# Performance work log

Hardware: AMD Instinct MI355X
Metric: run time of the kernel (lower is better)

Reference implementation:

```python
import jax, jax.numpy as jnp
from jax import lax
import numpy as np

T, N, E = 4, 50000, 1600000
IN_CH, HID, OUT = 128, 128, 16


def setup_inputs() -> dict:
    key = jax.random.key(0)
    ks = jax.random.split(key, 10)
    s = lambda fan: 1.0 / np.sqrt(fan)
    return {
        "xs": jax.random.normal(ks[0], (T, N, IN_CH), jnp.float32),
        "edges": jax.random.randint(ks[1], (T, 2, E), 0, N, dtype=jnp.int32),
        "W_gcn": jax.random.normal(ks[2], (HID, IN_CH), jnp.float32) * s(IN_CH),
        "b_gcn": jax.random.normal(ks[3], (HID,), jnp.float32) * s(IN_CH),
        "W_ih": jax.random.normal(ks[4], (3 * HID, HID), jnp.float32) * s(HID),
        "W_hh": jax.random.normal(ks[5], (3 * HID, HID), jnp.float32) * s(HID),
        "b_ih": jax.random.normal(ks[6], (3 * HID,), jnp.float32) * s(HID),
        "b_hh": jax.random.normal(ks[7], (3 * HID,), jnp.float32) * s(HID),
        "W_cls": jax.random.normal(ks[8], (OUT, HID), jnp.float32) * s(HID),
        "b_cls": jax.random.normal(ks[9], (OUT,), jnp.float32) * s(HID),
    }


def reference(xs, edges, W_gcn, b_gcn, W_ih, W_hh, b_ih, b_hh, W_cls, b_cls):
    n = xs.shape[1]
    loop = jnp.arange(n, dtype=edges.dtype)

    def gcn_forward(x, ei):
        src = jnp.concatenate([ei[0], loop])  # add self loops
        dst = jnp.concatenate([ei[1], loop])
        h = x @ W_gcn.T + b_gcn                               # [N, H]
        agg = jax.ops.segment_sum(h[src], dst, num_segments=n)  # scatter_add features
        deg = jax.ops.segment_sum(jnp.ones(dst.shape[0], h.dtype), dst, num_segments=n)
        return jax.nn.relu(agg / jnp.maximum(deg, 1.0)[:, None])

    def gru_cell(z, h):
        gi = z @ W_ih.T + b_ih   # [1, 3H]
        gh = h @ W_hh.T + b_hh
        ir, iz, ig = jnp.split(gi, 3, axis=1)
        hr, hz, hg = jnp.split(gh, 3, axis=1)
        r = jax.nn.sigmoid(ir + hr)
        zg = jax.nn.sigmoid(iz + hz)
        ng = jnp.tanh(ig + r * hg)
        return (1.0 - zg) * ng + zg * h

    def step(h, snap):
        x, ei = snap
        z_mean = gcn_forward(x, ei).mean(axis=0, keepdims=True)  # [1, H]
        return gru_cell(z_mean, h), None

    h0 = jnp.zeros((1, W_hh.shape[1]), xs.dtype)
    h, _ = lax.scan(step, h0, (xs, edges))
    return h @ W_cls.T + b_cls  # [1, OUT]
```

## Files before the change

kernel.cpp:

```cpp
#include <hip/hip_runtime.h>
#include <hip/hip_bf16.h>

typedef unsigned int u32;
typedef unsigned short u16;
typedef unsigned char u8;
typedef __attribute__((ext_vector_type(8))) __bf16 bfrag;
typedef __attribute__((ext_vector_type(4))) float f32x4;
typedef __attribute__((ext_vector_type(2))) float f32x2;

#define T_STEPS 4
#define N_NODES 50000
#define E_EDGES 1600000
#define HID 128
#define OUT_CH 16

#define NCHUNK 128
#define CHUNK (E_EDGES / NCHUNK)
#define NBKT 196
#define BCAP 10240

#define H_STRIDE    6400000u
#define RS_STRIDE   204800u
#define ZP_STRIDE   16384u
#define CSR_STRIDE  3200000u

#define OFF_H     0u
#define OFF_RS    25600000u
#define OFF_ZPAD  26419200u
#define OFF_CSR   26484736u
#define OFF_WB    39284736u
#define OFF_GCNT  39317504u
#define OFF_BBASE 39321600u
#define OFF_RECS  39325696u

__device__ __forceinline__ u8 f32_to_fp8(float v) {
    return (u8)(__builtin_amdgcn_cvt_pk_fp8_f32(v, v, 0, 0) & 0xFF);
}

__global__ void wbf_kernel(const float* __restrict__ W, __bf16* __restrict__ wb) {
    const int i = blockIdx.x * 256 + threadIdx.x;
    wb[i] = (__bf16)W[i];
}

__global__ __launch_bounds__(256) void gemm_mfma_kernel(const float* __restrict__ xs,
                                                        const __bf16* __restrict__ wb,
                                                        const float* __restrict__ b,
                                                        u8* __restrict__ h8_all) {
    const int lane = threadIdx.x & 63;
    const int wv   = threadIdx.x >> 6;
    const int r16  = lane & 15;
    const int quad = lane >> 4;
    const int mb   = blockIdx.x;
    const int t    = blockIdx.y;
    const float* x = xs + (size_t)t * N_NODES * 128;
    u8* h8         = h8_all + (size_t)t * H_STRIDE;

    bfrag Bf[2][4];
#pragma unroll
    for (int nt = 0; nt < 2; ++nt) {
        const int c = wv * 32 + nt * 16 + r16;
#pragma unroll
        for (int ks = 0; ks < 4; ++ks)
            Bf[nt][ks] = *(const bfrag*)(wb + c * 128 + ks * 32 + quad * 8);
    }

    const float* xp = x + (size_t)(mb * 16 + r16) * 128 + quad * 8;
    bfrag Af[4];
#pragma unroll
    for (int ks = 0; ks < 4; ++ks) {
        const float* ap = xp + ks * 32;
#pragma unroll
        for (int j = 0; j < 8; ++j) Af[ks][j] = (__bf16)ap[j];
    }

    f32x4 acc0 = {0.f, 0.f, 0.f, 0.f};
    f32x4 acc1 = {0.f, 0.f, 0.f, 0.f};
#pragma unroll
    for (int ks = 0; ks < 4; ++ks) {
        acc0 = __builtin_amdgcn_mfma_f32_16x16x32_bf16(Af[ks], Bf[0][ks], acc0, 0, 0, 0);
        acc1 = __builtin_amdgcn_mfma_f32_16x16x32_bf16(Af[ks], Bf[1][ks], acc1, 0, 0, 0);
    }

    const int c0 = wv * 32 + r16;
    const float b0 = b[c0], b1 = b[c0 + 16];
#pragma unroll
    for (int r = 0; r < 4; ++r) {
        const size_t row = (size_t)(mb * 16 + quad * 4 + r) * 128;
        h8[row + c0]      = f32_to_fp8(acc0[r] + b0);
        h8[row + c0 + 16] = f32_to_fp8(acc1[r] + b1);
    }
}

__global__ __launch_bounds__(256) void part_kernel(const int* __restrict__ edges,
                                                   u32* __restrict__ gcnt,
                                                   u32* __restrict__ recs) {
    __shared__ u32 bh[NBKT], bc[NBKT];
    const int id  = blockIdx.x;
    const int xcd = id & 7;
    const int t   = xcd >> 1;
    const int c   = ((xcd & 1) << 6) | (id >> 3);
    const int base = c * CHUNK;
    const int* src = edges + (size_t)t * 2 * E_EDGES;
    const int* dst = src + E_EDGES;
    u32* rt = recs + (size_t)t * NBKT * BCAP;
    const int tid = threadIdx.x;

    if (tid < NBKT) bh[tid] = 0;
    __syncthreads();
    for (int i = tid; i < CHUNK; i += 256)
        atomicAdd(&bh[dst[base + i] >> 8], 1u);
    __syncthreads();
    if (tid < NBKT) bc[tid] = atomicAdd(&gcnt[t * 256 + tid], bh[tid]);
    __syncthreads();
    for (int i = tid; i < CHUNK; i += 256) {
        const int d = dst[base + i];
        const int s = src[base + i];
        const int bkt = d >> 8;
        const u32 idx = atomicAdd(&bc[bkt], 1u);
        if (idx < (u32)BCAP)
            rt[(size_t)bkt * BCAP + idx] = ((u32)(d & 255) << 16) | (u32)s;
    }
}

__global__ __launch_bounds__(256) void bscan_kernel(const u32* __restrict__ gcnt,
                                                    u32* __restrict__ bbase) {
    __shared__ u32 sc[256];
    const int tid = threadIdx.x;
    for (int t = 0; t < T_STEPS; ++t) {
        u32 v = (tid < NBKT) ? min(gcnt[t * 256 + tid], (u32)BCAP) : 0u;
        const u32 mine = v;
        sc[tid] = v;
        __syncthreads();
        for (int d = 1; d < 256; d <<= 1) {
            const u32 u = (tid >= d) ? sc[tid - d] : 0u;
            __syncthreads();
            sc[tid] += u;
            __syncthreads();
        }
        if (tid < NBKT) bbase[t * 256 + tid] = sc[tid] - mine;
        __syncthreads();
    }
}

__global__ __launch_bounds__(256) void build_kernel(const u32* __restrict__ recs,
                                                    const u32* __restrict__ gcnt,
                                                    const u32* __restrict__ bbase,
                                                    int* __restrict__ rs_all,
                                                    u16* __restrict__ csr_all) {
    __shared__ u32 ncnt[256];
    __shared__ u32 ncur[256];
    __shared__ u16 cl[BCAP];
    const int id  = blockIdx.x;
    const int xcd = id & 7;
    const int t   = xcd >> 1;
    const int b   = ((xcd & 1) ? 98 : 0) + (id >> 3);
    const int tid = threadIdx.x;
    const u32 cnt   = min(gcnt[t * 256 + b], (u32)BCAP);
    const u32 rbase = bbase[t * 256 + b];
    const u32* rp = recs + ((size_t)t * NBKT + b) * BCAP;
    int* rs  = rs_all + (size_t)t * (RS_STRIDE / 4);
    u16* csr = csr_all + (size_t)t * (CSR_STRIDE / 2);

    ncnt[tid] = 0;
    __syncthreads();
    for (u32 i = tid; i < cnt; i += 256)
        atomicAdd(&ncnt[rp[i] >> 16], 1u);
    __syncthreads();
    const u32 mine = ncnt[tid];
    for (int d = 1; d < 256; d <<= 1) {
        const u32 v = (tid >= d) ? ncnt[tid - d] : 0u;
        __syncthreads();
        ncnt[tid] += v;
        __syncthreads();
    }
    const u32 off = ncnt[tid] - mine;
    ncur[tid] = off;
    const int n = b * 256 + tid;
    if (n <= N_NODES) rs[n] = (int)(rbase + off);
    __syncthreads();
    for (u32 i = tid; i < cnt; i += 256) {
        const u32 r = rp[i];
        const u32 p = atomicAdd(&ncur[r >> 16], 1u);
        cl[p] = (u16)(r & 0xFFFFu);
    }
    __syncthreads();
    for (u32 i = tid; i < cnt; i += 256)
        csr[rbase + i] = cl[i];
}

__global__ __launch_bounds__(256) void gather_kernel(const u32* __restrict__ h8_all,
                                                     const int* __restrict__ rs_all,
                                                     const u16* __restrict__ csr_all,
                                                     float* __restrict__ zp_all) {
    const int lane = threadIdx.x & 63;
    const int wv   = __builtin_amdgcn_readfirstlane((int)(threadIdx.x >> 6));
    const int q    = lane & 31;
    const bool h0  = lane < 32;
    const int o    = h0 ? 0 : 1;
    const int id   = blockIdx.x;
    const int xcd  = id & 7;
    const int t    = xcd >> 1;
    const int kb   = ((xcd & 1) << 10) | (id >> 3);
    const u32* h8d = h8_all + (size_t)t * (H_STRIDE / 4);
    const int* row_start = rs_all + (size_t)t * (RS_STRIDE / 4);
    const u16* csr = csr_all + (size_t)t * (CSR_STRIDE / 2);
    float* z_pad = zp_all + (size_t)t * (ZP_STRIDE / 4);
    const int gw   = kb * 4 + wv;
    const int nw   = 2048 * 4;

    float z0 = 0.f, z1 = 0.f, z2 = 0.f, z3 = 0.f;
    for (int n = gw; n < N_NODES; n += nw) {
        const int rs  = row_start[n];
        const int cnt = row_start[n + 1] - rs;
        const u32 us = h8d[n * 32 + q];
        const f32x2 slo = __builtin_amdgcn_cvt_pk_f32_fp8(us, 0);
        const f32x2 shi = __builtin_amdgcn_cvt_pk_f32_fp8(us, 1);
        float a0 = h0 ? slo.x : 0.f;
        float a1 = h0 ? slo.y : 0.f;
        float a2 = h0 ? shi.x : 0.f;
        float a3 = h0 ? shi.y : 0.f;

        const u16* lst = csr + rs;
        int i = 0;
        for (; i + 8 <= cnt; i += 8) {
            const int s0 = lst[i + 0 + o];
            const int s1 = lst[i + 2 + o];
            const int s2 = lst[i + 4 + o];
            const int s3 = lst[i + 6 + o];
            const u32 u0 = h8d[s0 * 32 + q];
            const u32 u1 = h8d[s1 * 32 + q];
            const u32 u2 = h8d[s2 * 32 + q];
            const u32 u3 = h8d[s3 * 32 + q];
            const f32x2 l0 = __builtin_amdgcn_cvt_pk_f32_fp8(u0, 0);
            const f32x2 g0 = __builtin_amdgcn_cvt_pk_f32_fp8(u0, 1);
            const f32x2 l1 = __builtin_amdgcn_cvt_pk_f32_fp8(u1, 0);
            const f32x2 g1 = __builtin_amdgcn_cvt_pk_f32_fp8(u1, 1);
            const f32x2 l2 = __builtin_amdgcn_cvt_pk_f32_fp8(u2, 0);
            const f32x2 g2 = __builtin_amdgcn_cvt_pk_f32_fp8(u2, 1);
            const f32x2 l3 = __builtin_amdgcn_cvt_pk_f32_fp8(u3, 0);
            const f32x2 g3 = __builtin_amdgcn_cvt_pk_f32_fp8(u3, 1);
            a0 += (l0.x + l1.x) + (l2.x + l3.x);
            a1 += (l0.y + l1.y) + (l2.y + l3.y);
            a2 += (g0.x + g1.x) + (g2.x + g3.x);
            a3 += (g0.y + g1.y) + (g2.y + g3.y);
        }
        for (; i + 2 <= cnt; i += 2) {
            const int s = lst[i + o];
            const u32 u = h8d[s * 32 + q];
            const f32x2 lo = __builtin_amdgcn_cvt_pk_f32_fp8(u, 0);
            const f32x2 hi = __builtin_amdgcn_cvt_pk_f32_fp8(u, 1);
            a0 += lo.x; a1 += lo.y; a2 += hi.x; a3 += hi.y;
        }
        if (i < cnt) {
            const int s = lst[i];
            const u32 u = h8d[s * 32 + q];
            const f32x2 lo = __builtin_amdgcn_cvt_pk_f32_fp8(u, 0);
            const f32x2 hi = __builtin_amdgcn_cvt_pk_f32_fp8(u, 1);
            if (h0) { a0 += lo.x; a1 += lo.y; a2 += hi.x; a3 += hi.y; }
        }
        a0 += __shfl_xor(a0, 32);
        a1 += __shfl_xor(a1, 32);
        a2 += __shfl_xor(a2, 32);
        a3 += __shfl_xor(a3, 32);
        const float inv = 1.0f / (float)(cnt + 1);
        z0 += fmaxf(a0 * inv, 0.f);
        z1 += fmaxf(a1 * inv, 0.f);
        z2 += fmaxf(a2 * inv, 0.f);
        z3 += fmaxf(a3 * inv, 0.f);
    }

    __shared__ float red[4][64][4];
    red[wv][lane][0] = z0;
    red[wv][lane][1] = z1;
    red[wv][lane][2] = z2;
    red[wv][lane][3] = z3;
    __syncthreads();
    if (threadIdx.x < 128) {
        const int c = threadIdx.x;
        const int g = c >> 2, m = c & 3;
        float s = 0.f;
#pragma unroll
        for (int w = 0; w < 4; ++w) s += red[w][g][m] + red[w][g + 32][m];
        atomicAdd(&z_pad[c * 32], 0.5f * s);
    }
}

__global__ __launch_bounds__(512) void gru_all_kernel(const float* __restrict__ zp_all,
                                                      const float* __restrict__ W_ih,
                                                      const float* __restrict__ W_hh,
                                                      const float* __restrict__ b_ih,
                                                      const float* __restrict__ b_hh,
                                                      const float* __restrict__ W_cls,
                                                      const float* __restrict__ b_cls,
                                                      float* __restrict__ out) {
    __shared__ float zm[128], hs[128], gi[384], gh[384];
    const int tid = threadIdx.x;
    if (tid < 128) hs[tid] = 0.f;
    for (int t = 0; t < T_STEPS; ++t) {
        if (tid < 128)
            zm[tid] = zp_all[(size_t)t * (ZP_STRIDE / 4) + tid * 32] * (1.0f / (float)N_NODES);
        __syncthreads();
        if (tid < 384) {
            float a = b_ih[tid], g = b_hh[tid];
            const float* wi = W_ih + tid * 128;
            const float* wh = W_hh + tid * 128;
#pragma unroll 8
            for (int k = 0; k < 128; ++k) {
                a = fmaf(zm[k], wi[k], a);
                g = fmaf(hs[k], wh[k], g);
            }
            gi[tid] = a;
            gh[tid] = g;
        }
        __syncthreads();
        if (tid < 128) {
            const float r  = 1.f / (1.f + expf(-(gi[tid] + gh[tid])));
            const float zg = 1.f / (1.f + expf(-(gi[128 + tid] + gh[128 + tid])));
            const float ng = tanhf(gi[256 + tid] + r * gh[256 + tid]);
            hs[tid] = (1.f - zg) * ng + zg * hs[tid];
        }
        __syncthreads();
    }
    if (tid < OUT_CH) {
        float a = b_cls[tid];
        const float* wc = W_cls + tid * 128;
#pragma unroll 8
        for (int k = 0; k < 128; ++k) a = fmaf(hs[k], wc[k], a);
        out[tid] = a;
    }
}

extern "C" void kernel_launch(void* const* d_in, const int* in_sizes, int n_in,
                              void* d_out, int out_size, void* d_ws, size_t ws_size,
                              hipStream_t stream) {
    const float* xs    = (const float*)d_in[0];
    const int*   edges = (const int*)d_in[1];
    const float* W_gcn = (const float*)d_in[2];
    const float* b_gcn = (const float*)d_in[3];
    const float* W_ih  = (const float*)d_in[4];
    const float* W_hh  = (const float*)d_in[5];
    const float* b_ih  = (const float*)d_in[6];
    const float* b_hh  = (const float*)d_in[7];
    const float* W_cls = (const float*)d_in[8];
    const float* b_cls = (const float*)d_in[9];
    float* out = (float*)d_out;

    char* ws = (char*)d_ws;
    u8*    h8        = (u8*)(ws + OFF_H);
    int*   row_start = (int*)(ws + OFF_RS);
    float* z_pad     = (float*)(ws + OFF_ZPAD);
    u16*   csr       = (u16*)(ws + OFF_CSR);
    __bf16* wb       = (__bf16*)(ws + OFF_WB);
    u32*   gcnt      = (u32*)(ws + OFF_GCNT);
    u32*   bbase     = (u32*)(ws + OFF_BBASE);
    u32*   recs      = (u32*)(ws + OFF_RECS);

    hipMemsetAsync(z_pad, 0, 4 * ZP_STRIDE, stream);
    hipMemsetAsync(gcnt, 0, 4096, stream);
    wbf_kernel<<<64, 256, 0, stream>>>(W_gcn, wb);

    gemm_mfma_kernel<<<dim3(3125, T_STEPS), 256, 0, stream>>>(xs, wb, b_gcn, h8);
    part_kernel<<<NCHUNK * T_STEPS, 256, 0, stream>>>(edges, gcnt, recs);
    bscan_kernel<<<1, 256, 0, stream>>>(gcnt, bbase);
    build_kernel<<<98 * 8, 256, 0, stream>>>(recs, gcnt, bbase, row_start, csr);
    gather_kernel<<<2048 * T_STEPS, 256, 0, stream>>>((const u32*)h8, row_start, csr, z_pad);
    gru_all_kernel<<<1, 512, 0, stream>>>(z_pad, W_ih, W_hh, b_ih, b_hh,
                                          W_cls, b_cls, out);
}
```

Measured before the change: 568.2 us.

## Split feature dimension across XCD halves and gather four edges per wave

```diff
diff --git a/kernel.cpp b/kernel.cpp
--- a/kernel.cpp
+++ b/kernel.cpp
@@ -194,43 +194,44 @@
                                                      float* __restrict__ zp_all) {
     const int lane = threadIdx.x & 63;
     const int wv   = __builtin_amdgcn_readfirstlane((int)(threadIdx.x >> 6));
-    const int q    = lane & 31;
-    const bool h0  = lane < 32;
-    const int o    = h0 ? 0 : 1;
+    const int qh   = lane & 15;
+    const int quar = lane >> 4;
     const int id   = blockIdx.x;
     const int xcd  = id & 7;
     const int t    = xcd >> 1;
-    const int kb   = ((xcd & 1) << 10) | (id >> 3);
-    const u32* h8d = h8_all + (size_t)t * (H_STRIDE / 4);
+    const int half = xcd & 1;
+    const int kb   = id >> 3;
+    const u32* h8d = h8_all + (size_t)t * (H_STRIDE / 4) + half * 16;
     const int* row_start = rs_all + (size_t)t * (RS_STRIDE / 4);
     const u16* csr = csr_all + (size_t)t * (CSR_STRIDE / 2);
     float* z_pad = zp_all + (size_t)t * (ZP_STRIDE / 4);
     const int gw   = kb * 4 + wv;
-    const int nw   = 2048 * 4;
+    const int nw   = 1024 * 4;
 
     float z0 = 0.f, z1 = 0.f, z2 = 0.f, z3 = 0.f;
     for (int n = gw; n < N_NODES; n += nw) {
         const int rs  = row_start[n];
         const int cnt = row_start[n + 1] - rs;
-        const u32 us = h8d[n * 32 + q];
+        const u32 us = h8d[n * 32 + qh];
         const f32x2 slo = __builtin_amdgcn_cvt_pk_f32_fp8(us, 0);
         const f32x2 shi = __builtin_amdgcn_cvt_pk_f32_fp8(us, 1);
-        float a0 = h0 ? slo.x : 0.f;
-        float a1 = h0 ? slo.y : 0.f;
-        float a2 = h0 ? shi.x : 0.f;
-        float a3 = h0 ? shi.y : 0.f;
+        const bool q0 = (quar == 0);
+        float a0 = q0 ? slo.x : 0.f;
+        float a1 = q0 ? slo.y : 0.f;
+        float a2 = q0 ? shi.x : 0.f;
+        float a3 = q0 ? shi.y : 0.f;
 
         const u16* lst = csr + rs;
         int i = 0;
-        for (; i + 8 <= cnt; i += 8) {
-            const int s0 = lst[i + 0 + o];
-            const int s1 = lst[i + 2 + o];
-            const int s2 = lst[i + 4 + o];
-            const int s3 = lst[i + 6 + o];
-            const u32 u0 = h8d[s0 * 32 + q];
-            const u32 u1 = h8d[s1 * 32 + q];
-            const u32 u2 = h8d[s2 * 32 + q];
-            const u32 u3 = h8d[s3 * 32 + q];
+        for (; i + 16 <= cnt; i += 16) {
+            const int s0 = lst[i + 0  + quar];
+            const int s1 = lst[i + 4  + quar];
+            const int s2 = lst[i + 8  + quar];
+            const int s3 = lst[i + 12 + quar];
+            const u32 u0 = h8d[s0 * 32 + qh];
+            const u32 u1 = h8d[s1 * 32 + qh];
+            const u32 u2 = h8d[s2 * 32 + qh];
+            const u32 u3 = h8d[s3 * 32 + qh];
             const f32x2 l0 = __builtin_amdgcn_cvt_pk_f32_fp8(u0, 0);
             const f32x2 g0 = __builtin_amdgcn_cvt_pk_f32_fp8(u0, 1);
             const f32x2 l1 = __builtin_amdgcn_cvt_pk_f32_fp8(u1, 0);
@@ -244,24 +245,24 @@
             a2 += (g0.x + g1.x) + (g2.x + g3.x);
             a3 += (g0.y + g1.y) + (g2.y + g3.y);
         }
-        for (; i + 2 <= cnt; i += 2) {
-            const int s = lst[i + o];
-            const u32 u = h8d[s * 32 + q];
+        for (; i + 4 <= cnt; i += 4) {
+            const int s = lst[i + quar];
+            const u32 u = h8d[s * 32 + qh];
             const f32x2 lo = __builtin_amdgcn_cvt_pk_f32_fp8(u, 0);
             const f32x2 hi = __builtin_amdgcn_cvt_pk_f32_fp8(u, 1);
             a0 += lo.x; a1 += lo.y; a2 += hi.x; a3 += hi.y;
         }
-        if (i < cnt) {
-            const int s = lst[i];
-            const u32 u = h8d[s * 32 + q];
+        if (quar < cnt - i) {
+            const int s = lst[i + quar];
+            const u32 u = h8d[s * 32 + qh];
             const f32x2 lo = __builtin_amdgcn_cvt_pk_f32_fp8(u, 0);
             const f32x2 hi = __builtin_amdgcn_cvt_pk_f32_fp8(u, 1);
-            if (h0) { a0 += lo.x; a1 += lo.y; a2 += hi.x; a3 += hi.y; }
-        }
-        a0 += __shfl_xor(a0, 32);
-        a1 += __shfl_xor(a1, 32);
-        a2 += __shfl_xor(a2, 32);
-        a3 += __shfl_xor(a3, 32);
+            a0 += lo.x; a1 += lo.y; a2 += hi.x; a3 += hi.y;
+        }
+        a0 += __shfl_xor(a0, 16); a0 += __shfl_xor(a0, 32);
+        a1 += __shfl_xor(a1, 16); a1 += __shfl_xor(a1, 32);
+        a2 += __shfl_xor(a2, 16); a2 += __shfl_xor(a2, 32);
+        a3 += __shfl_xor(a3, 16); a3 += __shfl_xor(a3, 32);
         const float inv = 1.0f / (float)(cnt + 1);
         z0 += fmaxf(a0 * inv, 0.f);
         z1 += fmaxf(a1 * inv, 0.f);
@@ -269,19 +270,21 @@
         z3 += fmaxf(a3 * inv, 0.f);
     }
 
-    __shared__ float red[4][64][4];
-    red[wv][lane][0] = z0;
-    red[wv][lane][1] = z1;
-    red[wv][lane][2] = z2;
-    red[wv][lane][3] = z3;
-    __syncthreads();
-    if (threadIdx.x < 128) {
+    __shared__ float red[4][16][4];
+    if (lane < 16) {
+        red[wv][lane][0] = z0;
+        red[wv][lane][1] = z1;
+        red[wv][lane][2] = z2;
+        red[wv][lane][3] = z3;
+    }
+    __syncthreads();
+    if (threadIdx.x < 64) {
         const int c = threadIdx.x;
         const int g = c >> 2, m = c & 3;
         float s = 0.f;
 #pragma unroll
-        for (int w = 0; w < 4; ++w) s += red[w][g][m] + red[w][g + 32][m];
-        atomicAdd(&z_pad[c * 32], 0.5f * s);
+        for (int w = 0; w < 4; ++w) s += red[w][g][m];
+        atomicAdd(&z_pad[(half * 64 + c) * 32], s);
     }
 }
 
```

New measurement: 612.8 us. 1.08x slower.
